# Optimization experiments

Hardware: AMD Instinct MI355X
Metric: run time of the kernel (lower is better)

Reference implementation:

```python
import jax, jax.numpy as jnp
import numpy as np

E = 1024  # emb_dim

def _xavier(k, fan_in, fan_out):
    lim = float(np.sqrt(6.0 / (fan_in + fan_out)))
    return jax.random.uniform(k, (fan_out, fan_in), jnp.float32, -lim, lim)

def setup_inputs() -> dict:
    key = jax.random.key(0)
    ks = jax.random.split(key, 12)
    B, S, H = 2, 2048, 16
    inp = {
        "query": jax.random.normal(ks[0], (B, S, E), jnp.float32),
        "key": jax.random.normal(ks[1], (B, S, E), jnp.float32),
        "value": jax.random.normal(ks[2], (B, S, E), jnp.float32),
        "mask": jax.random.bernoulli(ks[3], 0.5, (B, S, S)),
        "num_heads": H,
        "Wq": _xavier(ks[4], E, E), "bq": jnp.zeros((E,), jnp.float32),
        "Wk": _xavier(ks[5], E, E), "bk": jnp.zeros((E,), jnp.float32),
        "Wv": _xavier(ks[6], E, E), "bv": jnp.zeros((E,), jnp.float32),
        "Wo": _xavier(ks[7], E, E), "bo": jnp.zeros((E,), jnp.float32),
    }
    return inp

def reference(query, key, value, mask, num_heads, Wq, bq, Wk, bk, Wv, bv, Wo, bo):
    B, S, Emb = query.shape
    H = num_heads
    d = Emb // H
    scale = jnp.sqrt(jnp.asarray(d, query.dtype))

    def split_heads(x, W, b):
        x = x @ W.T + b                       # [B,S,E]
        x = x.reshape(B, S, H, d)             # view(B,-1,H,d)
        return jnp.transpose(x, (0, 2, 1, 3)) # [B,H,S,d]

    q = split_heads(query, Wq, bq)
    k = split_heads(key, Wk, bk)
    v = split_heads(value, Wv, bv)

    scores = jnp.einsum('bhqd,bhkd->bhqk', q, k) / scale  # [B,H,S,S]
    scores = jnp.where(mask[:, None, :, :], jnp.asarray(-1e18, scores.dtype), scores)
    attn = jax.nn.softmax(scores, axis=-1)                # [B,H,S,S]
    out = jnp.einsum('bhqk,bhkd->bhqd', attn, v)          # [B,H,S,d]

    # faithful replication of the original's (buggy) reshapes:
    # bmm output layout is [B*H, S, d]; viewed as (H, B, S, d), permuted (0,2,1,3),
    # then flattened to (B, S, H*d).
    out = out.reshape(B * H, S, d)
    out = out.reshape(H, B, S, d)
    out = jnp.transpose(out, (0, 2, 1, 3)).reshape(B, S, H * d)
    out = out @ Wo.T + bo
    return out, attn.reshape(B * H, S, S)
```

## Files before the change

kernel.cpp:

```cpp
#include <hip/hip_runtime.h>
#include <stdint.h>

typedef __attribute__((ext_vector_type(4))) float f32x4;
typedef __attribute__((ext_vector_type(8))) short short8;
typedef unsigned short u16;
typedef unsigned int u32;
typedef unsigned long long u64;

#define GLDS16(g, l) __builtin_amdgcn_global_load_lds( \
    (const __attribute__((address_space(1))) void*)(g), \
    (__attribute__((address_space(3))) void*)(l), 16, 0, 0)

#define ORDER_FENCE() asm volatile("" ::: "memory")

#if __has_builtin(__builtin_amdgcn_exp2f)
#define EXP2(x) __builtin_amdgcn_exp2f(x)
#else
#define EXP2(x) __expf(0.69314718056f * (x))
#endif

__device__ __forceinline__ u16 f2bf(float x) {
  u32 u = __float_as_uint(x);
  u += 0x7fffu + ((u >> 16) & 1u);
  return (u16)(u >> 16);
}

__global__ __launch_bounds__(256) void prep_kernel(
    const float* __restrict__ q, const float* __restrict__ k,
    const float* __restrict__ v, const int* __restrict__ mask,
    const float* __restrict__ Wq, const float* __restrict__ Wk,
    const float* __restrict__ Wv, const float* __restrict__ Wo,
    u16* __restrict__ X, u16* __restrict__ Wb, u64* __restrict__ mb)
{
  const size_t tid = (size_t)blockIdx.x * 256 + threadIdx.x;
  const size_t nth = (size_t)gridDim.x * 256;
  for (size_t i = tid; i < 3ull * 524288ull; i += nth) {
    const int a = (int)(i / 524288ull);
    const size_t j = i - (size_t)a * 524288ull;
    const float4* s4 = (const float4*)(a == 0 ? q : a == 1 ? k : v);
    float4 x = s4[2 * j], y = s4[2 * j + 1];
    uint4 o;
    o.x = (u32)f2bf(x.x) | ((u32)f2bf(x.y) << 16);
    o.y = (u32)f2bf(x.z) | ((u32)f2bf(x.w) << 16);
    o.z = (u32)f2bf(y.x) | ((u32)f2bf(y.y) << 16);
    o.w = (u32)f2bf(y.z) | ((u32)f2bf(y.w) << 16);
    ((uint4*)X)[i] = o;
  }
  for (size_t i = tid; i < 4ull * 131072ull; i += nth) {
    const int a = (int)(i / 131072ull);
    const size_t j = i - (size_t)a * 131072ull;
    const float4* s4 = (const float4*)(a == 0 ? Wq : a == 1 ? Wk : a == 2 ? Wv : Wo);
    float4 x = s4[2 * j], y = s4[2 * j + 1];
    uint4 o;
    o.x = (u32)f2bf(x.x) | ((u32)f2bf(x.y) << 16);
    o.y = (u32)f2bf(x.z) | ((u32)f2bf(x.w) << 16);
    o.z = (u32)f2bf(y.x) | ((u32)f2bf(y.y) << 16);
    o.w = (u32)f2bf(y.z) | ((u32)f2bf(y.w) << 16);
    ((uint4*)Wb)[i] = o;
  }
  const int lane = threadIdx.x & 63;
  const size_t wid = tid >> 6, nw = nth >> 6;
  for (size_t wi = wid; wi < 131072ull; wi += nw) {
    int mm = mask[wi * 64 + lane];
    u64 bal = __ballot(mm != 0);
    if (lane == 0) mb[wi] = bal;
  }
}

__global__ __launch_bounds__(256, 2) void gemm_qkv_kernel(
    const u16* __restrict__ X, const u16* __restrict__ W,
    const float* __restrict__ bq, const float* __restrict__ bk,
    const float* __restrict__ bv,
    u16* __restrict__ Qb, u16* __restrict__ Kb, u16* __restrict__ Vt)
{
  const int z = blockIdx.z;
  const char* A = (const char*)(X + (size_t)z * 4194304ull);
  const char* B = (const char*)(W + (size_t)z * 1048576ull);
  const float* bias = (z == 0) ? bq : (z == 1) ? bk : bv;
  const int m0 = blockIdx.y * 128, n0 = blockIdx.x * 128;
  const int tid = threadIdx.x, l = tid & 63, w = tid >> 6;
  const int wm = w >> 1, wn = w & 1;
  __shared__ __attribute__((aligned(16))) char SM[32768];
  char* Asm = SM;
  char* Bsm = SM + 16384;
  f32x4 acc[4][4] = {};
  for (int kt = 0; kt < 16; ++kt) {
#pragma unroll
    for (int j = 0; j < 4; ++j) {
      const int rt = w * 32 + j * 8 + (l >> 3);
      const int swk = ((l & 7) * 16) ^ ((rt & 7) << 4);
      GLDS16(A + (size_t)(m0 + rt) * 2048 + kt * 128 + swk, Asm + (w * 32 + j * 8) * 128);
      GLDS16(B + (size_t)(n0 + rt) * 2048 + kt * 128 + swk, Bsm + (w * 32 + j * 8) * 128);
    }
    __syncthreads();
#pragma unroll
    for (int kk = 0; kk < 2; ++kk) {
      short8 af[4], bfr[4];
#pragma unroll
      for (int mf = 0; mf < 4; ++mf) {
        const int row = wm * 64 + mf * 16 + (l & 15);
        const int kb = kk * 64 + (l >> 4) * 16;
        af[mf] = *(const short8*)(Asm + row * 128 + (kb ^ ((row & 7) << 4)));
      }
#pragma unroll
      for (int fc = 0; fc < 4; ++fc) {
        const int row = wn * 64 + fc * 16 + (l & 15);
        const int kb = kk * 64 + (l >> 4) * 16;
        bfr[fc] = *(const short8*)(Bsm + row * 128 + (kb ^ ((row & 7) << 4)));
      }
#pragma unroll
      for (int mf = 0; mf < 4; ++mf)
#pragma unroll
        for (int fc = 0; fc < 4; ++fc)
          acc[mf][fc] = __builtin_amdgcn_mfma_f32_16x16x32_bf16(af[mf], bfr[fc], acc[mf][fc], 0, 0, 0);
    }
    __syncthreads();
  }
  if (z < 2) {
    const float scale = (z == 0) ? 0.18033688011f : 1.0f;
    u16* dst = (z == 0) ? Qb : Kb;
#pragma unroll
    for (int mf = 0; mf < 4; ++mf)
#pragma unroll
      for (int fc = 0; fc < 4; ++fc)
#pragma unroll
        for (int r = 0; r < 4; ++r) {
          const int m = m0 + wm * 64 + mf * 16 + (l >> 4) * 4 + r;
          const int n = n0 + wn * 64 + fc * 16 + (l & 15);
          const float val = (acc[mf][fc][r] + bias[n]) * scale;
          const int bb = m >> 11, s = m & 2047;
          const int hh = n >> 6, dd = n & 63;
          dst[((size_t)(bb * 16 + hh) * 2048 + s) * 64 + dd] = f2bf(val);
        }
  } else {
#pragma unroll
    for (int mf = 0; mf < 4; ++mf)
#pragma unroll
      for (int fc = 0; fc < 4; ++fc)
#pragma unroll
        for (int r = 0; r < 4; ++r) {
          const int n_l = wn * 64 + fc * 16 + (l & 15);
          const int m_l = wm * 64 + mf * 16 + (l >> 4) * 4 + r;
          const float val = acc[mf][fc][r] + bias[n0 + n_l];
          *(u16*)(SM + n_l * 256 + ((m_l * 2) ^ ((n_l & 15) << 4))) = f2bf(val);
        }
    __syncthreads();
    const int bb = m0 >> 11, ms = m0 & 2047;
#pragma unroll
    for (int rep = 0; rep < 8; ++rep) {
      const int n_l = rep * 16 + (tid >> 4);
      const int m8 = (tid & 15) * 8;
      const uint4 dv = *(const uint4*)(SM + n_l * 256 + ((m8 * 2) ^ ((n_l & 15) << 4)));
      const int hh = (n0 + n_l) >> 6, dd = (n0 + n_l) & 63;
      *(uint4*)(Vt + ((size_t)((bb * 16 + hh) * 64 + dd)) * 2048 + ms + m8) = dv;
    }
  }
}

__global__ __launch_bounds__(256, 4) void lsum_kernel(
    const u16* __restrict__ Qb, const u16* __restrict__ Kb,
    const u32* __restrict__ mbits, float* __restrict__ lrow)
{
  const int bh = blockIdx.y, qb = blockIdx.x;
  const int b = bh >> 4;
  const int q0 = qb * 64;
  const int tid = threadIdx.x, l = tid & 63, w = tid >> 6;

  __shared__ __attribute__((aligned(16))) char kbuf[2][16384];
  __shared__ float rbuf[4][64];

  const char* Qrow = (const char*)(Qb + (size_t)bh * 131072ull);
  const char* Krow = (const char*)(Kb + (size_t)bh * 131072ull);

  short8 aq[4][2];
#pragma unroll
  for (int qf = 0; qf < 4; ++qf)
#pragma unroll
    for (int kk = 0; kk < 2; ++kk)
      aq[qf][kk] = *(const short8*)(Qrow + (size_t)(q0 + qf * 16 + (l & 15)) * 128 +
                                    kk * 64 + (l >> 4) * 16);
  const u32* mbase[4];
#pragma unroll
  for (int qf = 0; qf < 4; ++qf)
    mbase[qf] = mbits + (size_t)(b * 2048 + q0 + qf * 16 + (l & 15)) * 64 + w;

  ORDER_FENCE();
#pragma unroll
  for (int j = 0; j < 4; ++j) {
    const int row = j * 32 + w * 8 + (l >> 3);
    GLDS16(Krow + (size_t)row * 128 + (((l & 7) * 16) ^ ((row & 7) << 4)),
           kbuf[0] + j * 4096 + w * 1024);
  }
  ORDER_FENCE();
  u32 mreg[4];
#pragma unroll
  for (int qf = 0; qf < 4; ++qf) mreg[qf] = mbase[qf][0];

  float lsum[4] = {0.f, 0.f, 0.f, 0.f};
  for (int t = 0; t < 16; ++t) {
    asm volatile("s_waitcnt vmcnt(4) lgkmcnt(0)" ::: "memory");
    __builtin_amdgcn_s_barrier();
    u32 mnext[4] = {0, 0, 0, 0};
    if (t < 15) {
      ORDER_FENCE();
#pragma unroll
      for (int j = 0; j < 4; ++j) {
        const int row = j * 32 + w * 8 + (l >> 3);
        GLDS16(Krow + (size_t)((t + 1) * 128 + row) * 128 + (((l & 7) * 16) ^ ((row & 7) << 4)),
               kbuf[(t + 1) & 1] + j * 4096 + w * 1024);
      }
      ORDER_FENCE();
#pragma unroll
      for (int qf = 0; qf < 4; ++qf) mnext[qf] = mbase[qf][(t + 1) * 4];
    }
#pragma unroll
    for (int i = 0; i < 2; ++i) {
      const int krow = (w * 2 + i) * 16 + (l & 15);
      short8 ak[2];
#pragma unroll
      for (int kk = 0; kk < 2; ++kk)
        ak[kk] = *(const short8*)(kbuf[t & 1] + krow * 128 +
                                  ((kk * 64 + (l >> 4) * 16) ^ ((krow & 7) << 4)));
#pragma unroll
      for (int qf = 0; qf < 4; ++qf) {
        f32x4 sc = {0.f, 0.f, 0.f, 0.f};
        sc = __builtin_amdgcn_mfma_f32_16x16x32_bf16(ak[0], aq[qf][0], sc, 0, 0, 0);
        sc = __builtin_amdgcn_mfma_f32_16x16x32_bf16(ak[1], aq[qf][1], sc, 0, 0, 0);
        const int bp = i * 16 + (l >> 4) * 4;
        float s = 0.f;
#pragma unroll
        for (int r = 0; r < 4; ++r)
          s += ((mreg[qf] >> (bp + r)) & 1u) ? 0.f : EXP2(sc[r]);
        lsum[qf] += s;
      }
    }
#pragma unroll
    for (int qf = 0; qf < 4; ++qf) mreg[qf] = mnext[qf];
  }
#pragma unroll
  for (int qf = 0; qf < 4; ++qf) {
    float v = lsum[qf];
    v += __shfl_xor(v, 16);
    v += __shfl_xor(v, 32);
    if (l < 16) rbuf[w][qf * 16 + l] = v;
  }
  __syncthreads();
  if (tid < 64)
    lrow[(size_t)bh * 2048 + q0 + tid] =
        rbuf[0][tid] + rbuf[1][tid] + rbuf[2][tid] + rbuf[3][tid];
}

__global__ __launch_bounds__(512, 4) void attn_kernel(
    const u16* __restrict__ Qb, const u16* __restrict__ Kb,
    const u16* __restrict__ Vt, const u32* __restrict__ mbits,
    const float* __restrict__ lrow, float* __restrict__ attn,
    u16* __restrict__ preWo)
{
  const int bh = blockIdx.y, qb = blockIdx.x;
  const int b = bh >> 4, h = bh & 15;
  const int q0 = qb * 128;
  const int tid = threadIdx.x, l = tid & 63, w = tid >> 6;
  const int wk = w & 3, wqh = w >> 2;
  const int wq = w >> 1, wd = w & 1;

  __shared__ __attribute__((aligned(16))) char kbuf[2][8192];
  __shared__ __attribute__((aligned(16))) char vbuf[2][8192];
  __shared__ __attribute__((aligned(16))) char Psm[16384];

  const char* Qrow = (const char*)(Qb + (size_t)bh * 131072ull);
  const char* Krow = (const char*)(Kb + (size_t)bh * 131072ull);
  const char* Vrow = (const char*)(Vt + (size_t)bh * 131072ull);

  {
    const int row = tid >> 3, byte = (tid & 7) * 16;
    GLDS16(Qrow + (size_t)(q0 + row) * 128 + (byte ^ ((row & 7) << 4)), Psm + w * 1024);
    const int row2 = 64 + row;
    GLDS16(Qrow + (size_t)(q0 + row2) * 128 + (byte ^ ((row2 & 7) << 4)), Psm + 8192 + w * 1024);
    GLDS16(Krow + (size_t)row * 128 + (byte ^ ((row & 7) << 4)), kbuf[0] + w * 1024);
    GLDS16(Vrow + (size_t)row * 4096 + (byte ^ ((row & 7) << 4)), vbuf[0] + w * 1024);
  }
  __syncthreads();
  short8 aq[4][2];
#pragma unroll
  for (int qf = 0; qf < 4; ++qf)
#pragma unroll
    for (int kk = 0; kk < 2; ++kk) {
      const int row = wqh * 64 + qf * 16 + (l & 15);
      aq[qf][kk] = *(const short8*)(Psm + row * 128 +
                                    ((kk * 64 + (l >> 4) * 16) ^ ((row & 7) << 4)));
    }
  float il[4];
#pragma unroll
  for (int qf = 0; qf < 4; ++qf) {
    const float lv = lrow[(size_t)bh * 2048 + q0 + wqh * 64 + qf * 16 + (l & 15)];
    il[qf] = (lv > 0.f) ? 1.0f / lv : 0.f;
  }
  __syncthreads();

  const u32* mbase[4];
#pragma unroll
  for (int qf = 0; qf < 4; ++qf)
    mbase[qf] = mbits + (size_t)(b * 2048 + q0 + wqh * 64 + qf * 16 + (l & 15)) * 64 + (wk >> 1);
  u32 mreg[4];
#pragma unroll
  for (int qf = 0; qf < 4; ++qf) mreg[qf] = mbase[qf][0];

  f32x4 oacc[2][2] = {};
  const int kbit = (wk & 1) * 16 + (l >> 4) * 4;
  for (int t = 0; t < 32; ++t) {
    asm volatile("s_waitcnt vmcnt(8) lgkmcnt(0)" ::: "memory");
    __builtin_amdgcn_s_barrier();
    u32 mnext[4] = {0, 0, 0, 0};
    if (t < 31) {
      const int row = tid >> 3, byte = (tid & 7) * 16;
      ORDER_FENCE();
      GLDS16(Krow + (size_t)((t + 1) * 64 + row) * 128 + (byte ^ ((row & 7) << 4)),
             kbuf[(t + 1) & 1] + w * 1024);
      GLDS16(Vrow + (size_t)row * 4096 + (t + 1) * 128 + (byte ^ ((row & 7) << 4)),
             vbuf[(t + 1) & 1] + w * 1024);
      ORDER_FENCE();
#pragma unroll
      for (int qf = 0; qf < 4; ++qf) mnext[qf] = mbase[qf][(t + 1) * 2];
      ORDER_FENCE();
    }
    short8 ak[2];
    {
      const int krow = wk * 16 + (l & 15);
      ak[0] = *(const short8*)(kbuf[t & 1] + krow * 128 +
                               (((l >> 4) * 16) ^ ((krow & 7) << 4)));
      ak[1] = *(const short8*)(kbuf[t & 1] + krow * 128 +
                               ((64 + (l >> 4) * 16) ^ ((krow & 7) << 4)));
    }
#pragma unroll
    for (int qf = 0; qf < 4; ++qf) {
      f32x4 sc = {0.f, 0.f, 0.f, 0.f};
      sc = __builtin_amdgcn_mfma_f32_16x16x32_bf16(ak[0], aq[qf][0], sc, 0, 0, 0);
      sc = __builtin_amdgcn_mfma_f32_16x16x32_bf16(ak[1], aq[qf][1], sc, 0, 0, 0);
      const int q = wqh * 64 + qf * 16 + (l & 15);
      float p[4];
#pragma unroll
      for (int r = 0; r < 4; ++r)
        p[r] = ((mreg[qf] >> (kbit + r)) & 1u) ? 0.f : EXP2(sc[r]) * il[qf];
      uint2 pk;
      pk.x = (u32)f2bf(p[0]) | ((u32)f2bf(p[1]) << 16);
      pk.y = (u32)f2bf(p[2]) | ((u32)f2bf(p[3]) << 16);
      *(uint2*)(Psm + q * 128 + ((wk * 32 + (l >> 4) * 8) ^ ((q & 7) << 4))) = pk;
    }
#pragma unroll
    for (int qf = 0; qf < 4; ++qf) mreg[qf] = mnext[qf];
    asm volatile("s_waitcnt lgkmcnt(0)" ::: "memory");
    __builtin_amdgcn_s_barrier();
#pragma unroll
    for (int it = 0; it < 4; ++it) {
      const int q = w * 16 + it * 4 + (l >> 4);
      const uint2 pv = *(const uint2*)(Psm + q * 128 + (((l & 15) * 8) ^ ((q & 7) << 4)));
      f32x4 o;
      o[0] = __uint_as_float(pv.x << 16);
      o[1] = __uint_as_float(pv.x & 0xffff0000u);
      o[2] = __uint_as_float(pv.y << 16);
      o[3] = __uint_as_float(pv.y & 0xffff0000u);
      __builtin_nontemporal_store(o, (f32x4*)(attn +
          ((size_t)bh * 2048 + q0 + q) * 2048 + t * 64 + (l & 15) * 4));
    }
#pragma unroll
    for (int ka = 0; ka < 2; ++ka) {
      short8 pa[2], vb[2];
#pragma unroll
      for (int i = 0; i < 2; ++i) {
        const int qr = wq * 32 + i * 16 + (l & 15);
        pa[i] = *(const short8*)(Psm + qr * 128 +
                                 ((ka * 64 + (l >> 4) * 16) ^ ((qr & 7) << 4)));
      }
#pragma unroll
      for (int j = 0; j < 2; ++j) {
        const int dr = wd * 32 + j * 16 + (l & 15);
        vb[j] = *(const short8*)(vbuf[t & 1] + dr * 128 +
                                 ((ka * 64 + (l >> 4) * 16) ^ ((dr & 7) << 4)));
      }
#pragma unroll
      for (int i = 0; i < 2; ++i)
#pragma unroll
        for (int j = 0; j < 2; ++j)
          oacc[i][j] = __builtin_amdgcn_mfma_f32_16x16x32_bf16(pa[i], vb[j], oacc[i][j], 0, 0, 0);
    }
  }

#pragma unroll
  for (int i = 0; i < 2; ++i)
#pragma unroll
    for (int j = 0; j < 2; ++j)
#pragma unroll
      for (int r = 0; r < 4; ++r) {
        const int qg = q0 + wq * 32 + i * 16 + (l >> 4) * 4 + r;
        const int dd = wd * 32 + j * 16 + (l & 15);
        const size_t off = (size_t)b * 2097152ull +
                           ((size_t)((h >> 1) * 256 + (qg >> 3))) * 1024ull +
                           (size_t)((qg & 7) * 128 + (h & 1) * 64 + dd);
        preWo[off] = f2bf(oacc[i][j][r]);
      }
}

__global__ __launch_bounds__(256, 2) void gemm_out_kernel(
    const u16* __restrict__ A0, const u16* __restrict__ B0,
    const float* __restrict__ bias, float* __restrict__ out)
{
  const char* A = (const char*)A0;
  const char* B = (const char*)B0;
  const int m0 = blockIdx.y * 128, n0 = blockIdx.x * 128;
  const int tid = threadIdx.x, l = tid & 63, w = tid >> 6;
  const int wm = w >> 1, wn = w & 1;
  __shared__ __attribute__((aligned(16))) char SM[32768];
  char* Asm = SM;
  char* Bsm = SM + 16384;
  f32x4 acc[4][4] = {};
  for (int kt = 0; kt < 16; ++kt) {
#pragma unroll
    for (int j = 0; j < 4; ++j) {
      const int rt = w * 32 + j * 8 + (l >> 3);
      const int swk = ((l & 7) * 16) ^ ((rt & 7) << 4);
      GLDS16(A + (size_t)(m0 + rt) * 2048 + kt * 128 + swk, Asm + (w * 32 + j * 8) * 128);
      GLDS16(B + (size_t)(n0 + rt) * 2048 + kt * 128 + swk, Bsm + (w * 32 + j * 8) * 128);
    }
    __syncthreads();
#pragma unroll
    for (int kk = 0; kk < 2; ++kk) {
      short8 af[4], bfr[4];
#pragma unroll
      for (int mf = 0; mf < 4; ++mf) {
        const int row = wm * 64 + mf * 16 + (l & 15);
        const int kb = kk * 64 + (l >> 4) * 16;
        af[mf] = *(const short8*)(Asm + row * 128 + (kb ^ ((row & 7) << 4)));
      }
#pragma unroll
      for (int fc = 0; fc < 4; ++fc) {
        const int row = wn * 64 + fc * 16 + (l & 15);
        const int kb = kk * 64 + (l >> 4) * 16;
        bfr[fc] = *(const short8*)(Bsm + row * 128 + (kb ^ ((row & 7) << 4)));
      }
#pragma unroll
      for (int mf = 0; mf < 4; ++mf)
#pragma unroll
        for (int fc = 0; fc < 4; ++fc)
          acc[mf][fc] = __builtin_amdgcn_mfma_f32_16x16x32_bf16(af[mf], bfr[fc], acc[mf][fc], 0, 0, 0);
    }
    __syncthreads();
  }
#pragma unroll
  for (int mf = 0; mf < 4; ++mf)
#pragma unroll
    for (int fc = 0; fc < 4; ++fc)
#pragma unroll
      for (int r = 0; r < 4; ++r) {
        const int m = m0 + wm * 64 + mf * 16 + (l >> 4) * 4 + r;
        const int n = n0 + wn * 64 + fc * 16 + (l & 15);
        out[(size_t)m * 1024 + n] = acc[mf][fc][r] + bias[n];
      }
}

extern "C" void kernel_launch(void* const* d_in, const int* in_sizes, int n_in,
                              void* d_out, int out_size, void* d_ws, size_t ws_size,
                              hipStream_t stream) {
  const float* q  = (const float*)d_in[0];
  const float* k  = (const float*)d_in[1];
  const float* v  = (const float*)d_in[2];
  const int*  mask = (const int*)d_in[3];
  const float* Wq = (const float*)d_in[5];
  const float* bq = (const float*)d_in[6];
  const float* Wk = (const float*)d_in[7];
  const float* bk = (const float*)d_in[8];
  const float* Wv = (const float*)d_in[9];
  const float* bv = (const float*)d_in[10];
  const float* Wo = (const float*)d_in[11];
  const float* bo = (const float*)d_in[12];

  float* out0 = (float*)d_out;
  float* attn = out0 + 4194304;
  u16* X = (u16*)attn;
  char* ws = (char*)d_ws;
  u16* Qb    = (u16*)(ws);
  u16* Kb    = (u16*)(ws + 8388608);
  u16* Vt    = (u16*)(ws + 16777216);
  u16* preWo = (u16*)(ws + 25165824);
  u16* Wb    = (u16*)(ws + 33554432);
  u32* mbits = (u32*)(ws + 41943040);
  float* lrow = (float*)(ws + 33554432);

  prep_kernel<<<dim3(1024), 256, 0, stream>>>(q, k, v, mask, Wq, Wk, Wv, Wo,
                                              X, Wb, (u64*)mbits);
  gemm_qkv_kernel<<<dim3(8, 32, 3), 256, 0, stream>>>(X, Wb, bq, bk, bv, Qb, Kb, Vt);
  lsum_kernel<<<dim3(32, 32), 256, 0, stream>>>(Qb, Kb, mbits, lrow);
  attn_kernel<<<dim3(16, 32), 512, 0, stream>>>(Qb, Kb, Vt, mbits, lrow, attn, preWo);
  gemm_out_kernel<<<dim3(8, 32), 256, 0, stream>>>(preWo, Wb + 3u * 1048576u, bo, out0);
}
```

Baseline: 272.8 us.

## Software-pipeline attention loop: defer PV and attn store by one tile

New measurement: 263.1 us. 1.04x faster.

```diff
diff --git a/kernel.cpp b/kernel.cpp
--- a/kernel.cpp
+++ b/kernel.cpp
@@ -264,8 +264,8 @@
   const int wq = w >> 1, wd = w & 1;
 
   __shared__ __attribute__((aligned(16))) char kbuf[2][8192];
-  __shared__ __attribute__((aligned(16))) char vbuf[2][8192];
-  __shared__ __attribute__((aligned(16))) char Psm[16384];
+  __shared__ __attribute__((aligned(16))) char vbuf[3][8192];
+  __shared__ __attribute__((aligned(16))) char Psm[2][16384];
 
   const char* Qrow = (const char*)(Qb + (size_t)bh * 131072ull);
   const char* Krow = (const char*)(Kb + (size_t)bh * 131072ull);
@@ -273,9 +273,9 @@
 
   {
     const int row = tid >> 3, byte = (tid & 7) * 16;
-    GLDS16(Qrow + (size_t)(q0 + row) * 128 + (byte ^ ((row & 7) << 4)), Psm + w * 1024);
+    GLDS16(Qrow + (size_t)(q0 + row) * 128 + (byte ^ ((row & 7) << 4)), Psm[0] + w * 1024);
     const int row2 = 64 + row;
-    GLDS16(Qrow + (size_t)(q0 + row2) * 128 + (byte ^ ((row2 & 7) << 4)), Psm + 8192 + w * 1024);
+    GLDS16(Qrow + (size_t)(q0 + row2) * 128 + (byte ^ ((row2 & 7) << 4)), Psm[0] + 8192 + w * 1024);
     GLDS16(Krow + (size_t)row * 128 + (byte ^ ((row & 7) << 4)), kbuf[0] + w * 1024);
     GLDS16(Vrow + (size_t)row * 4096 + (byte ^ ((row & 7) << 4)), vbuf[0] + w * 1024);
   }
@@ -286,7 +286,7 @@
 #pragma unroll
     for (int kk = 0; kk < 2; ++kk) {
       const int row = wqh * 64 + qf * 16 + (l & 15);
-      aq[qf][kk] = *(const short8*)(Psm + row * 128 +
+      aq[qf][kk] = *(const short8*)(Psm[0] + row * 128 +
                                     ((kk * 64 + (l >> 4) * 16) ^ ((row & 7) << 4)));
     }
   float il[4];
@@ -307,9 +307,15 @@
 
   f32x4 oacc[2][2] = {};
   const int kbit = (wk & 1) * 16 + (l >> 4) * 4;
+  int vstage = 1, vprev = 2;
   for (int t = 0; t < 32; ++t) {
-    asm volatile("s_waitcnt vmcnt(8) lgkmcnt(0)" ::: "memory");
-    __builtin_amdgcn_s_barrier();
+    if (t == 1) {
+      asm volatile("s_waitcnt vmcnt(4) lgkmcnt(0)" ::: "memory");
+      __builtin_amdgcn_s_barrier();
+    } else if (t >= 2) {
+      asm volatile("s_waitcnt vmcnt(8) lgkmcnt(0)" ::: "memory");
+      __builtin_amdgcn_s_barrier();
+    }
     u32 mnext[4] = {0, 0, 0, 0};
     if (t < 31) {
       const int row = tid >> 3, byte = (tid & 7) * 16;
@@ -317,11 +323,26 @@
       GLDS16(Krow + (size_t)((t + 1) * 64 + row) * 128 + (byte ^ ((row & 7) << 4)),
              kbuf[(t + 1) & 1] + w * 1024);
       GLDS16(Vrow + (size_t)row * 4096 + (t + 1) * 128 + (byte ^ ((row & 7) << 4)),
-             vbuf[(t + 1) & 1] + w * 1024);
+             vbuf[vstage] + w * 1024);
       ORDER_FENCE();
 #pragma unroll
       for (int qf = 0; qf < 4; ++qf) mnext[qf] = mbase[qf][(t + 1) * 2];
       ORDER_FENCE();
+    }
+    if (t > 0) {
+      const char* Pp = Psm[(t - 1) & 1];
+#pragma unroll
+      for (int it = 0; it < 4; ++it) {
+        const int q = w * 16 + it * 4 + (l >> 4);
+        const uint2 pv = *(const uint2*)(Pp + q * 128 + (((l & 15) * 8) ^ ((q & 7) << 4)));
+        f32x4 o;
+        o[0] = __uint_as_float(pv.x << 16);
+        o[1] = __uint_as_float(pv.x & 0xffff0000u);
+        o[2] = __uint_as_float(pv.y << 16);
+        o[3] = __uint_as_float(pv.y & 0xffff0000u);
+        __builtin_nontemporal_store(o, (f32x4*)(attn +
+            ((size_t)bh * 2048 + q0 + q) * 2048 + (t - 1) * 64 + (l & 15) * 4));
+      }
     }
     short8 ak[2];
     {
@@ -344,23 +365,53 @@
       uint2 pk;
       pk.x = (u32)f2bf(p[0]) | ((u32)f2bf(p[1]) << 16);
       pk.y = (u32)f2bf(p[2]) | ((u32)f2bf(p[3]) << 16);
-      *(uint2*)(Psm + q * 128 + ((wk * 32 + (l >> 4) * 8) ^ ((q & 7) << 4))) = pk;
+      *(uint2*)(Psm[t & 1] + q * 128 + ((wk * 32 + (l >> 4) * 8) ^ ((q & 7) << 4))) = pk;
     }
 #pragma unroll
     for (int qf = 0; qf < 4; ++qf) mreg[qf] = mnext[qf];
-    asm volatile("s_waitcnt lgkmcnt(0)" ::: "memory");
-    __builtin_amdgcn_s_barrier();
+    if (t > 0) {
+      const char* Pp = Psm[(t - 1) & 1];
+#pragma unroll
+      for (int ka = 0; ka < 2; ++ka) {
+        short8 pa[2], vb[2];
+#pragma unroll
+        for (int i = 0; i < 2; ++i) {
+          const int qr = wq * 32 + i * 16 + (l & 15);
+          pa[i] = *(const short8*)(Pp + qr * 128 +
+                                   ((ka * 64 + (l >> 4) * 16) ^ ((qr & 7) << 4)));
+        }
+#pragma unroll
+        for (int j = 0; j < 2; ++j) {
+          const int dr = wd * 32 + j * 16 + (l & 15);
+          vb[j] = *(const short8*)(vbuf[vprev] + dr * 128 +
+                                   ((ka * 64 + (l >> 4) * 16) ^ ((dr & 7) << 4)));
+        }
+#pragma unroll
+        for (int i = 0; i < 2; ++i)
+#pragma unroll
+          for (int j = 0; j < 2; ++j)
+            oacc[i][j] = __builtin_amdgcn_mfma_f32_16x16x32_bf16(pa[i], vb[j], oacc[i][j], 0, 0, 0);
+      }
+    }
+    vstage = (vstage == 2) ? 0 : vstage + 1;
+    vprev = (vprev == 2) ? 0 : vprev + 1;
+  }
+
+  asm volatile("s_waitcnt lgkmcnt(0)" ::: "memory");
+  __builtin_amdgcn_s_barrier();
+  {
+    const char* Pp = Psm[1];
 #pragma unroll
     for (int it = 0; it < 4; ++it) {
       const int q = w * 16 + it * 4 + (l >> 4);
-      const uint2 pv = *(const uint2*)(Psm + q * 128 + (((l & 15) * 8) ^ ((q & 7) << 4)));
+      const uint2 pv = *(const uint2*)(Pp + q * 128 + (((l & 15) * 8) ^ ((q & 7) << 4)));
       f32x4 o;
       o[0] = __uint_as_float(pv.x << 16);
       o[1] = __uint_as_float(pv.x & 0xffff0000u);
       o[2] = __uint_as_float(pv.y << 16);
       o[3] = __uint_as_float(pv.y & 0xffff0000u);
       __builtin_nontemporal_store(o, (f32x4*)(attn +
-          ((size_t)bh * 2048 + q0 + q) * 2048 + t * 64 + (l & 15) * 4));
+          ((size_t)bh * 2048 + q0 + q) * 2048 + 31 * 64 + (l & 15) * 4));
     }
 #pragma unroll
     for (int ka = 0; ka < 2; ++ka) {
@@ -368,13 +419,13 @@
 #pragma unroll
       for (int i = 0; i < 2; ++i) {
         const int qr = wq * 32 + i * 16 + (l & 15);
-        pa[i] = *(const short8*)(Psm + qr * 128 +
+        pa[i] = *(const short8*)(Pp + qr * 128 +
                                  ((ka * 64 + (l >> 4) * 16) ^ ((qr & 7) << 4)));
       }
 #pragma unroll
       for (int j = 0; j < 2; ++j) {
         const int dr = wd * 32 + j * 16 + (l & 15);
-        vb[j] = *(const short8*)(vbuf[t & 1] + dr * 128 +
+        vb[j] = *(const short8*)(vbuf[1] + dr * 128 +
                                  ((ka * 64 + (l >> 4) * 16) ^ ((dr & 7) << 4)));
       }
 #pragma unroll
```
